# Optimization experiments

Hardware: AMD Instinct MI355X
Metric: run time of the kernel (lower is better)

## Reference

```python
import jax, jax.numpy as jnp
import numpy as np
import math

EMBED_DIM = 2048
NUM_HEADS = 16
HEAD_DIM = EMBED_DIM // NUM_HEADS
BATCH = 2
SEQ = 2048


def setup_inputs() -> dict:
    key = jax.random.key(0)
    ks = jax.random.split(key, 6)
    scale = 1.0 / math.sqrt(EMBED_DIM)
    x = jax.random.normal(ks[0], (BATCH, SEQ, EMBED_DIM), dtype=jnp.float32)
    mask = jnp.ones((BATCH, SEQ), dtype=jnp.float32)
    Wq = jax.random.normal(ks[1], (EMBED_DIM, EMBED_DIM), dtype=jnp.float32) * scale
    Wk = jax.random.normal(ks[2], (EMBED_DIM, EMBED_DIM), dtype=jnp.float32) * scale
    Wv = jax.random.normal(ks[3], (EMBED_DIM, EMBED_DIM), dtype=jnp.float32) * scale
    Wo = jax.random.normal(ks[4], (EMBED_DIM, EMBED_DIM), dtype=jnp.float32) * scale
    return {"x": x, "mask": mask, "Wq": Wq, "Wk": Wk, "Wv": Wv, "Wo": Wo}


def _rope(q, k, seq_len):
    # q, k: [B, H, S, D]
    d = q.shape[-1]
    position = jnp.arange(seq_len, dtype=jnp.float32)[:, None]          # [S,1]
    freqs = 1.0 / (10000.0 ** (jnp.arange(0, d, 2, dtype=jnp.float32) / d))  # [D/2]
    angles = position * freqs                                            # [S,D/2]
    sin = jnp.concatenate([jnp.sin(angles), jnp.sin(angles)], axis=-1)[None, None]  # [1,1,S,D]
    cos = jnp.concatenate([jnp.cos(angles), jnp.cos(angles)], axis=-1)[None, None]

    def rotate_half(t):
        t1, t2 = jnp.split(t, 2, axis=-1)
        return jnp.concatenate([-t2, t1], axis=-1)

    q = q * cos + rotate_half(q) * sin
    k = k * cos + rotate_half(k) * sin
    return q, k


def reference(x, mask, Wq, Wk, Wv, Wo):
    B, S, E = x.shape
    H, D = NUM_HEADS, HEAD_DIM
    # nn.Linear(y) = y @ W.T
    q = (x @ Wq.T).reshape(B, S, H, D).transpose(0, 2, 1, 3)  # [B,H,S,D]
    k = (x @ Wk.T).reshape(B, S, H, D).transpose(0, 2, 1, 3)
    v = (x @ Wv.T).reshape(B, S, H, D).transpose(0, 2, 1, 3)
    q, k = _rope(q, k, S)
    scores = jnp.einsum('bhqd,bhkd->bhqk', q, k) / math.sqrt(D)  # [B,H,S,S]
    # causal mask (strict upper triangle -> -inf)
    causal = jnp.triu(jnp.full((S, S), -jnp.inf, dtype=scores.dtype), k=1)
    scores = scores + causal[None, None]
    # padding mask: [B,S] -> [B,1,1,S] over keys
    scores = scores + (1.0 - mask)[:, None, None, :] * -1e9
    attn = jax.nn.softmax(scores, axis=-1)
    context = jnp.einsum('bhqk,bhkd->bhqd', attn, v)  # [B,H,S,D]
    context = context.transpose(0, 2, 1, 3).reshape(B, S, E)
    return context @ Wo.T
```

## Files before the change

### kernel.cpp

```cpp
#include <hip/hip_runtime.h>
#include <math.h>

typedef unsigned short u16;
typedef __attribute__((ext_vector_type(8))) short bf16x8;
typedef __attribute__((ext_vector_type(8))) unsigned short u16x8;
typedef __attribute__((ext_vector_type(4))) float f32x4;

#define MFMA(a, b, c) __builtin_amdgcn_mfma_f32_16x16x32_bf16((a), (b), (c), 0, 0, 0)

#define GLOAD_LDS16(g, l)                                                     \
  __builtin_amdgcn_global_load_lds(                                           \
      (const __attribute__((address_space(1))) void*)(g),                     \
      (__attribute__((address_space(3))) void*)(l), 16, 0, 0)

#define DRAIN_VMEM() asm volatile("s_waitcnt vmcnt(0)" ::: "memory")
#define FENCE_LDS()                                                            \
  do {                                                                         \
    asm volatile("s_waitcnt lgkmcnt(0)" ::: "memory");                         \
    __builtin_amdgcn_sched_barrier(0);                                         \
  } while (0)

__device__ __forceinline__ float bf2f(u16 u) {
  union { unsigned int i; float f; } x; x.i = ((unsigned int)u) << 16; return x.f;
}
__device__ __forceinline__ u16 f2bf(float f) {
  union { float f; unsigned int i; } x; x.f = f;
  unsigned int r = x.i + 0x7FFFu + ((x.i >> 16) & 1u);
  return (u16)(r >> 16);
}

__global__ __launch_bounds__(256) void probe_all(const u16* p0, const u16* p1,
                                                 const u16* p2, const u16* p3,
                                                 const u16* p4, const u16* p5,
                                                 int* __restrict__ flags) {
  const u16* ps[6] = {p0, p1, p2, p3, p4, p5};
  const u16* p = ps[blockIdx.x];
  __shared__ int cnt;
  if (threadIdx.x == 0) cnt = 0;
  __syncthreads();
  const u16 u = p[threadIdx.x * 2];
  const int e = (u >> 7) & 0xFF;
  atomicAdd(&cnt, (e >= 110 && e <= 135) ? 1 : 0);
  __syncthreads();
  if (threadIdx.x == 0) flags[blockIdx.x] = (cnt > 128) ? 1 : 0;
}

__global__ __launch_bounds__(256) void convert_to_bf16(const void* __restrict__ in,
                                                       u16* __restrict__ out, int n8,
                                                       const int* __restrict__ flag) {
  const int i = blockIdx.x * 256 + threadIdx.x;
  if (i >= n8) return;
  if (*flag) {
    ((u16x8*)out)[i] = ((const u16x8*)in)[i];
  } else {
    const float* f = (const float*)in + (size_t)i * 8;
    u16x8 r;
#pragma unroll
    for (int j = 0; j < 8; ++j) r[j] = f2bf(f[j]);
    ((u16x8*)out)[i] = r;
  }
}

__global__ __launch_bounds__(256) void build_mexp(const void* __restrict__ mask,
                                                  const int* __restrict__ mflag,
                                                  float* __restrict__ mexp, int n) {
  const int i = blockIdx.x * 256 + threadIdx.x;
  if (i >= n) return;
  const float m = *mflag ? bf2f(((const u16*)mask)[i]) : ((const float*)mask)[i];
  mexp[i] = (1.0f - m) * -1e9f;
}

__global__ __launch_bounds__(256) void gemm_bt(const u16* __restrict__ A,
                                               const u16* __restrict__ B,
                                               void* __restrict__ dst,
                                               int K, int mode) {
  __shared__ __align__(16) u16 As[2][128 * 64];
  __shared__ __align__(16) u16 Bs[2][128 * 64];
  const int tid  = threadIdx.x;
  const int wave = tid >> 6, lane = tid & 63;
  const int quad = lane >> 4, m16 = lane & 15;
  const int wm = (wave >> 1) * 64, wn = (wave & 1) * 64;
  const size_t bi = (size_t)blockIdx.y * 128;
  const size_t bj = (size_t)blockIdx.x * 128;

  f32x4 acc[4][4];
  const f32x4 fz = {0.f, 0.f, 0.f, 0.f};
#pragma unroll
  for (int i = 0; i < 4; ++i)
#pragma unroll
    for (int j = 0; j < 4; ++j) acc[i][j] = fz;

  const u16* gA[4]; const u16* gB[4]; int lofs[4];
#pragma unroll
  for (int j = 0; j < 4; ++j) {
    const int t  = (wave * 4 + j) * 64 + lane;
    const int r  = t >> 3;
    const int cs = t & 7;
    const int c  = cs ^ (r & 7);
    gA[j] = A + (bi + r) * (size_t)K + c * 8;
    gB[j] = B + (bj + r) * (size_t)K + c * 8;
    lofs[j] = t * 8;
  }

#pragma unroll
  for (int j = 0; j < 4; ++j) GLOAD_LDS16(gA[j], &As[0][lofs[j]]);
#pragma unroll
  for (int j = 0; j < 4; ++j) GLOAD_LDS16(gB[j], &Bs[0][lofs[j]]);

  const int nIter = K >> 6;
  for (int it = 0; it < nIter; ++it) {
    DRAIN_VMEM();
    __syncthreads();
    if (it + 1 < nIter) {
      const int ko = (it + 1) << 6;
      const int nb = (it + 1) & 1;
#pragma unroll
      for (int j = 0; j < 4; ++j) GLOAD_LDS16(gA[j] + ko, &As[nb][lofs[j]]);
#pragma unroll
      for (int j = 0; j < 4; ++j) GLOAD_LDS16(gB[j] + ko, &Bs[nb][lofs[j]]);
    }
    const int cb = it & 1;

    bf16x8 af[2][4], bfv[2][4];
#pragma unroll
    for (int kk = 0; kk < 2; ++kk) {
#pragma unroll
      for (int mt = 0; mt < 4; ++mt) {
        const int m = wm + mt * 16 + m16;
        af[kk][mt] = *(const bf16x8*)&As[cb][m * 64 + ((kk * 4 + quad) ^ (m & 7)) * 8];
      }
#pragma unroll
      for (int nt = 0; nt < 4; ++nt) {
        const int n = wn + nt * 16 + m16;
        bfv[kk][nt] = *(const bf16x8*)&Bs[cb][n * 64 + ((kk * 4 + quad) ^ (n & 7)) * 8];
      }
    }
#pragma unroll
    for (int kk = 0; kk < 2; ++kk)
#pragma unroll
      for (int mt = 0; mt < 4; ++mt)
#pragma unroll
        for (int nt = 0; nt < 4; ++nt)
          acc[mt][nt] = MFMA(af[kk][mt], bfv[kk][nt], acc[mt][nt]);
  }

#pragma unroll
  for (int mt = 0; mt < 4; ++mt) {
#pragma unroll
    for (int nt = 0; nt < 4; ++nt) {
#pragma unroll
      for (int rg = 0; rg < 4; ++rg) {
        const int row = (int)bi + wm + mt * 16 + quad * 4 + rg;
        const int col = (int)bj + wn + nt * 16 + m16;
        const float v = acc[mt][nt][rg];
        if (mode == 2) {
          ((float*)dst)[(size_t)row * 2048 + col] = v;
        } else {
          const int bb = row >> 11, s = row & 2047, hh = col >> 7, dd = col & 127;
          const size_t idx =
              (mode == 0) ? ((((size_t)bb * 16 + hh) * 2048 + s) * 128 + dd)
                          : ((((size_t)bb * 16 + hh) * 128 + dd) * 2048 + s);
          ((u16*)dst)[idx] = f2bf(v);
        }
      }
    }
  }
}

__global__ __launch_bounds__(256) void rope_kernel(u16* __restrict__ Qr,
                                                   u16* __restrict__ Kr) {
  const int tid = blockIdx.x * 256 + threadIdx.x;
  const int j  = tid & 63;
  const int s  = (tid >> 6) & 2047;
  const int bh = tid >> 17;
  const size_t base = ((size_t)bh * 2048 + s) * 128;
  const float freq = __expf(-(float)j * (9.2103403719761836f / 64.0f));
  float sn, cs;
  sincosf((float)s * freq, &sn, &cs);
  const float qs = 0.08838834764831845f;
  const float q1 = bf2f(Qr[base + j]), q2 = bf2f(Qr[base + j + 64]);
  Qr[base + j]      = f2bf((q1 * cs - q2 * sn) * qs);
  Qr[base + j + 64] = f2bf((q2 * cs + q1 * sn) * qs);
  const float k1 = bf2f(Kr[base + j]), k2 = bf2f(Kr[base + j + 64]);
  Kr[base + j]      = f2bf(k1 * cs - k2 * sn);
  Kr[base + j + 64] = f2bf(k2 * cs + k1 * sn);
}

__global__ __launch_bounds__(256, 2) void flash_attn(const u16* __restrict__ Q,
                                                     const u16* __restrict__ Kg,
                                                     const u16* __restrict__ Vg,
                                                     const float* __restrict__ mexp_g,
                                                     u16* __restrict__ ctx) {
  const int S = 2048, D = 128;
  __shared__ __align__(16) u16 Kt[2][64 * 128];
  __shared__ __align__(16) u16 Vt[2][128 * 64];
  __shared__ __align__(16) u16 Pt[128 * 64];
  const int tid  = threadIdx.x;
  const int wave = tid >> 6, lane = tid & 63;
  const int quad = lane >> 4, m16 = lane & 15;
  const int qtile = 15 - (int)blockIdx.x;
  const int q0 = qtile * 128;
  const int bh = blockIdx.y;
  const int b = bh >> 4, h = bh & 15;
  const size_t baseQK = (size_t)bh * S * D;
  const size_t baseV  = (size_t)bh * D * S;

  const u16* gK[4]; const u16* gV[4]; int lK[4], lV[4];
#pragma unroll
  for (int j = 0; j < 4; ++j) {
    const int t = (wave * 4 + j) * 64 + lane;
    {
      const int r = t >> 4, cs = t & 15;
      const int c = (cs & 8) | ((cs ^ r) & 7);
      gK[j] = Kg + baseQK + (size_t)r * D + c * 8;
      lK[j] = t * 8;
    }
    {
      const int d = t >> 3, cs = t & 7;
      const int c = cs ^ (d & 7);
      gV[j] = Vg + baseV + (size_t)d * S + c * 8;
      lV[j] = t * 8;
    }
  }

  bf16x8 qf[2][4];
#pragma unroll
  for (int st = 0; st < 2; ++st)
#pragma unroll
    for (int kb = 0; kb < 4; ++kb)
      qf[st][kb] = *(const bf16x8*)&Q[baseQK +
          (size_t)(q0 + wave * 32 + st * 16 + m16) * D + kb * 32 + quad * 8];

  float li[2][4] = {{0.f, 0.f, 0.f, 0.f}, {0.f, 0.f, 0.f, 0.f}};
  f32x4 oacc[2][8];
  const f32x4 fz = {0.f, 0.f, 0.f, 0.f};
#pragma unroll
  for (int st = 0; st < 2; ++st)
#pragma unroll
    for (int dt = 0; dt < 8; ++dt) oacc[st][dt] = fz;

#pragma unroll
  for (int j = 0; j < 4; ++j) GLOAD_LDS16(gK[j], &Kt[0][lK[j]]);
#pragma unroll
  for (int j = 0; j < 4; ++j) GLOAD_LDS16(gV[j], &Vt[0][lV[j]]);

  const int ktmax = 2 * qtile + 1;
  for (int kt = 0; kt <= ktmax; ++kt) {
    const int k0 = kt * 64;
    const int cb = kt & 1;
    DRAIN_VMEM();
    __syncthreads();

    float madd[4];
#pragma unroll
    for (int nt = 0; nt < 4; ++nt)
      madd[nt] = mexp_g[b * S + k0 + nt * 16 + m16];

    if (kt < ktmax) {
      const int nb = 1 - cb;
#pragma unroll
      for (int j = 0; j < 4; ++j) GLOAD_LDS16(gK[j] + (size_t)(k0 + 64) * D, &Kt[nb][lK[j]]);
#pragma unroll
      for (int j = 0; j < 4; ++j) GLOAD_LDS16(gV[j] + (k0 + 64), &Vt[nb][lV[j]]);
    }

#pragma unroll
    for (int st = 0; st < 2; ++st) {
      f32x4 sacc[4];
#pragma unroll
      for (int nt = 0; nt < 4; ++nt) sacc[nt] = fz;
#pragma unroll
      for (int nt = 0; nt < 4; ++nt)
#pragma unroll
        for (int kb = 0; kb < 4; ++kb) {
          const int c = kb * 4 + quad;
          const int cs = (c & 8) | ((c ^ m16) & 7);
          bf16x8 kf = *(const bf16x8*)&Kt[cb][(nt * 16 + m16) * 128 + cs * 8];
          sacc[nt] = MFMA(qf[st][kb], kf, sacc[nt]);
        }

      const int R0   = q0 + wave * 32 + st * 16;
      const int prow = wave * 32 + st * 16 + quad * 4;
      if (k0 + 63 > R0) {
#pragma unroll
        for (int rg = 0; rg < 4; ++rg) {
          const int row = R0 + quad * 4 + rg;
          const int pr  = prow + rg;
          float ps = 0.f;
#pragma unroll
          for (int nt = 0; nt < 4; ++nt) {
            const int col = k0 + nt * 16 + m16;
            const float p = (col > row) ? 0.f : __expf(sacc[nt][rg] + madd[nt]);
            ps += p;
            const int c = nt * 2 + (m16 >> 3);
            Pt[pr * 64 + ((c ^ pr) & 7) * 8 + (m16 & 7)] = f2bf(p);
          }
          li[st][rg] += ps;
        }
      } else {
#pragma unroll
        for (int rg = 0; rg < 4; ++rg) {
          const int pr = prow + rg;
          float ps = 0.f;
#pragma unroll
          for (int nt = 0; nt < 4; ++nt) {
            const float p = __expf(sacc[nt][rg] + madd[nt]);
            ps += p;
            const int c = nt * 2 + (m16 >> 3);
            Pt[pr * 64 + ((c ^ pr) & 7) * 8 + (m16 & 7)] = f2bf(p);
          }
          li[st][rg] += ps;
        }
      }
    }
    FENCE_LDS();

#pragma unroll
    for (int kb = 0; kb < 2; ++kb) {
      const int c = kb * 4 + quad;
      const int cs = (c ^ m16) & 7;
      bf16x8 pf0 = *(const bf16x8*)&Pt[(wave * 32 + m16) * 64 + cs * 8];
      bf16x8 pf1 = *(const bf16x8*)&Pt[(wave * 32 + 16 + m16) * 64 + cs * 8];
#pragma unroll
      for (int dt = 0; dt < 8; ++dt) {
        bf16x8 vf = *(const bf16x8*)&Vt[cb][(dt * 16 + m16) * 64 + cs * 8];
        oacc[0][dt] = MFMA(pf0, vf, oacc[0][dt]);
        oacc[1][dt] = MFMA(pf1, vf, oacc[1][dt]);
      }
    }
  }

#pragma unroll
  for (int st = 0; st < 2; ++st) {
#pragma unroll
    for (int rg = 0; rg < 4; ++rg) {
      float ls = li[st][rg];
#pragma unroll
      for (int mk = 1; mk < 16; mk <<= 1) ls += __shfl_xor(ls, mk, 64);
      const float inv = 1.0f / ls;
      const int srow = q0 + wave * 32 + st * 16 + quad * 4 + rg;
#pragma unroll
      for (int dt = 0; dt < 8; ++dt) {
        const int e = h * 128 + dt * 16 + m16;
        ctx[((size_t)b * S + srow) * 2048 + e] = f2bf(oacc[st][dt][rg] * inv);
      }
    }
  }
}

extern "C" void kernel_launch(void* const* d_in, const int* in_sizes, int n_in,
                              void* d_out, int out_size, void* d_ws, size_t ws_size,
                              hipStream_t stream) {
  (void)in_sizes; (void)n_in; (void)out_size; (void)ws_size;
  const int Bz = 2, S = 2048, E = 2048, H = 16, M = Bz * S;
  const size_t NX = (size_t)Bz * S * E;
  const size_t NW = (size_t)E * E;
  const size_t NM = (size_t)Bz * S;

  char* ws = (char*)d_ws;
  int*   flags = (int*)ws;
  float* mexp  = (float*)(ws + 256);
  u16* xc  = (u16*)(ws + 256 + 16384);
  u16* Wqc = xc + NX;
  u16* Wkc = Wqc + NW;
  u16* Wvc = Wkc + NW;
  u16* Woc = Wvc + NW;
  u16* Qr  = Woc + NW;
  u16* Kr  = Qr + NX;
  u16* Vt  = Kr + NX;
  u16* ctx = Vt + NX;

  probe_all<<<6, 256, 0, stream>>>((const u16*)d_in[0], (const u16*)d_in[1],
                                   (const u16*)d_in[2], (const u16*)d_in[3],
                                   (const u16*)d_in[4], (const u16*)d_in[5], flags);

  convert_to_bf16<<<(int)(NX / 8 / 256), 256, 0, stream>>>(d_in[0], xc,  (int)(NX / 8), flags + 0);
  convert_to_bf16<<<(int)(NW / 8 / 256), 256, 0, stream>>>(d_in[2], Wqc, (int)(NW / 8), flags + 2);
  convert_to_bf16<<<(int)(NW / 8 / 256), 256, 0, stream>>>(d_in[3], Wkc, (int)(NW / 8), flags + 3);
  convert_to_bf16<<<(int)(NW / 8 / 256), 256, 0, stream>>>(d_in[4], Wvc, (int)(NW / 8), flags + 4);
  convert_to_bf16<<<(int)(NW / 8 / 256), 256, 0, stream>>>(d_in[5], Woc, (int)(NW / 8), flags + 5);
  build_mexp<<<16, 256, 0, stream>>>(d_in[1], flags + 1, mexp, (int)NM);

  dim3 ggrid(E / 128, M / 128);
  gemm_bt<<<ggrid, 256, 0, stream>>>(xc, Wqc, Qr, E, 0);
  gemm_bt<<<ggrid, 256, 0, stream>>>(xc, Wkc, Kr, E, 0);
  gemm_bt<<<ggrid, 256, 0, stream>>>(xc, Wvc, Vt, E, 1);
  rope_kernel<<<(Bz * H * S * 64) / 256, 256, 0, stream>>>(Qr, Kr);
  flash_attn<<<dim3(16, Bz * H), 256, 0, stream>>>(Qr, Kr, Vt, mexp, ctx);
  gemm_bt<<<ggrid, 256, 0, stream>>>(ctx, Woc, d_out, E, 2);
}
```

Baseline: 439.7 us.

## Fuse input conversions and QKV GEMMs; restructure flash attention into balanced paired passes

Merges the five bf16 conversions and the mask build into one prep kernel. It also fuses the Q, K and V projections into a single GEMM launch over a concatenated weight matrix, with band-dependent output layout. Flash attention now gives each block two 64-row query halves from complementary tiles (a high and a low tile) to balance causal work. It also single-buffers V, with V loads overlapping the QK MFMA, and shrinks LDS use. The aim is fewer launches, better load balance and better occupancy, at the cost of less V prefetch depth.

```diff
diff --git a/kernel.cpp b/kernel.cpp
--- a/kernel.cpp
+++ b/kernel.cpp
@@ -45,29 +45,43 @@
   if (threadIdx.x == 0) flags[blockIdx.x] = (cnt > 128) ? 1 : 0;
 }
 
-__global__ __launch_bounds__(256) void convert_to_bf16(const void* __restrict__ in,
-                                                       u16* __restrict__ out, int n8,
-                                                       const int* __restrict__ flag) {
-  const int i = blockIdx.x * 256 + threadIdx.x;
-  if (i >= n8) return;
-  if (*flag) {
-    ((u16x8*)out)[i] = ((const u16x8*)in)[i];
+__global__ __launch_bounds__(256) void prep_all(const void* __restrict__ x_in,
+                                                const void* __restrict__ wq_in,
+                                                const void* __restrict__ wk_in,
+                                                const void* __restrict__ wv_in,
+                                                const void* __restrict__ wo_in,
+                                                const void* __restrict__ mask_in,
+                                                u16* __restrict__ xc,
+                                                float* __restrict__ mexp,
+                                                const int* __restrict__ flags) {
+  const int blk = blockIdx.x;
+  if (blk < 12288) {
+    const int i = blk * 256 + threadIdx.x;
+    const void* in; u16* out; int fi, off;
+    if (i < (1 << 20)) {
+      in = x_in; out = xc; fi = 0; off = i;
+    } else {
+      const int k = i - (1 << 20);
+      const int seg = k >> 19;
+      off = k & ((1 << 19) - 1);
+      in = (seg == 0) ? wq_in : (seg == 1) ? wk_in : (seg == 2) ? wv_in : wo_in;
+      out = xc + ((size_t)1 << 23) + ((size_t)seg << 22);
+      fi = 2 + seg;
+    }
+    if (flags[fi]) {
+      ((u16x8*)out)[off] = ((const u16x8*)in)[off];
+    } else {
+      const float* f = (const float*)in + (size_t)off * 8;
+      u16x8 r;
+#pragma unroll
+      for (int j = 0; j < 8; ++j) r[j] = f2bf(f[j]);
+      ((u16x8*)out)[off] = r;
+    }
   } else {
-    const float* f = (const float*)in + (size_t)i * 8;
-    u16x8 r;
-#pragma unroll
-    for (int j = 0; j < 8; ++j) r[j] = f2bf(f[j]);
-    ((u16x8*)out)[i] = r;
-  }
-}
-
-__global__ __launch_bounds__(256) void build_mexp(const void* __restrict__ mask,
-                                                  const int* __restrict__ mflag,
-                                                  float* __restrict__ mexp, int n) {
-  const int i = blockIdx.x * 256 + threadIdx.x;
-  if (i >= n) return;
-  const float m = *mflag ? bf2f(((const u16*)mask)[i]) : ((const float*)mask)[i];
-  mexp[i] = (1.0f - m) * -1e9f;
+    const int i = (blk - 12288) * 256 + threadIdx.x;
+    const float m = flags[1] ? bf2f(((const u16*)mask_in)[i]) : ((const float*)mask_in)[i];
+    mexp[i] = (1.0f - m) * -1e9f;
+  }
 }
 
 __global__ __launch_bounds__(256) void gemm_bt(const u16* __restrict__ A,
@@ -156,10 +170,12 @@
         if (mode == 2) {
           ((float*)dst)[(size_t)row * 2048 + col] = v;
         } else {
-          const int bb = row >> 11, s = row & 2047, hh = col >> 7, dd = col & 127;
-          const size_t idx =
-              (mode == 0) ? ((((size_t)bb * 16 + hh) * 2048 + s) * 128 + dd)
-                          : ((((size_t)bb * 16 + hh) * 128 + dd) * 2048 + s);
+          const int band = col >> 11, lc = col & 2047;
+          const int bb = row >> 11, s = row & 2047, hh = lc >> 7, dd = lc & 127;
+          const size_t bandbase = (size_t)band * 8388608u;
+          const size_t idx = (band == 2)
+              ? bandbase + ((((size_t)bb * 16 + hh) * 128 + dd) * 2048 + s)
+              : bandbase + ((((size_t)bb * 16 + hh) * 2048 + s) * 128 + dd);
           ((u16*)dst)[idx] = f2bf(v);
         }
       }
@@ -193,13 +209,13 @@
                                                      u16* __restrict__ ctx) {
   const int S = 2048, D = 128;
   __shared__ __align__(16) u16 Kt[2][64 * 128];
-  __shared__ __align__(16) u16 Vt[2][128 * 64];
-  __shared__ __align__(16) u16 Pt[128 * 64];
+  __shared__ __align__(16) u16 Vt[128 * 64];
+  __shared__ __align__(16) u16 Pt[64 * 64];
   const int tid  = threadIdx.x;
   const int wave = tid >> 6, lane = tid & 63;
   const int quad = lane >> 4, m16 = lane & 15;
-  const int qtile = 15 - (int)blockIdx.x;
-  const int q0 = qtile * 128;
+  const int px = blockIdx.x >> 1;
+  const int hl = blockIdx.x & 1;
   const int bh = blockIdx.y;
   const int b = bh >> 4, h = bh & 15;
   const size_t baseQK = (size_t)bh * S * D;
@@ -223,49 +239,47 @@
     }
   }
 
-  bf16x8 qf[2][4];
-#pragma unroll
-  for (int st = 0; st < 2; ++st)
+  const f32x4 fz = {0.f, 0.f, 0.f, 0.f};
+
+  for (int pass = 0; pass < 2; ++pass) {
+    const int qtile = pass ? px : 15 - px;
+    const int q0 = qtile * 128 + hl * 64;
+    const int ktmax = 2 * qtile + hl;
+
+    __syncthreads();
+
+    bf16x8 qf[4];
 #pragma unroll
     for (int kb = 0; kb < 4; ++kb)
-      qf[st][kb] = *(const bf16x8*)&Q[baseQK +
-          (size_t)(q0 + wave * 32 + st * 16 + m16) * D + kb * 32 + quad * 8];
-
-  float li[2][4] = {{0.f, 0.f, 0.f, 0.f}, {0.f, 0.f, 0.f, 0.f}};
-  f32x4 oacc[2][8];
-  const f32x4 fz = {0.f, 0.f, 0.f, 0.f};
-#pragma unroll
-  for (int st = 0; st < 2; ++st)
-#pragma unroll
-    for (int dt = 0; dt < 8; ++dt) oacc[st][dt] = fz;
-
-#pragma unroll
-  for (int j = 0; j < 4; ++j) GLOAD_LDS16(gK[j], &Kt[0][lK[j]]);
-#pragma unroll
-  for (int j = 0; j < 4; ++j) GLOAD_LDS16(gV[j], &Vt[0][lV[j]]);
-
-  const int ktmax = 2 * qtile + 1;
-  for (int kt = 0; kt <= ktmax; ++kt) {
-    const int k0 = kt * 64;
-    const int cb = kt & 1;
-    DRAIN_VMEM();
-    __syncthreads();
-
-    float madd[4];
-#pragma unroll
-    for (int nt = 0; nt < 4; ++nt)
-      madd[nt] = mexp_g[b * S + k0 + nt * 16 + m16];
-
-    if (kt < ktmax) {
-      const int nb = 1 - cb;
-#pragma unroll
-      for (int j = 0; j < 4; ++j) GLOAD_LDS16(gK[j] + (size_t)(k0 + 64) * D, &Kt[nb][lK[j]]);
-#pragma unroll
-      for (int j = 0; j < 4; ++j) GLOAD_LDS16(gV[j] + (k0 + 64), &Vt[nb][lV[j]]);
-    }
-
-#pragma unroll
-    for (int st = 0; st < 2; ++st) {
+      qf[kb] = *(const bf16x8*)&Q[baseQK +
+          (size_t)(q0 + wave * 16 + m16) * D + kb * 32 + quad * 8];
+
+    float li[4] = {0.f, 0.f, 0.f, 0.f};
+    f32x4 oacc[8];
+#pragma unroll
+    for (int dt = 0; dt < 8; ++dt) oacc[dt] = fz;
+
+#pragma unroll
+    for (int j = 0; j < 4; ++j) GLOAD_LDS16(gK[j], &Kt[0][lK[j]]);
+
+    for (int kt = 0; kt <= ktmax; ++kt) {
+      const int k0 = kt * 64;
+      const int cb = kt & 1;
+      DRAIN_VMEM();
+      __syncthreads();
+
+#pragma unroll
+      for (int j = 0; j < 4; ++j) GLOAD_LDS16(gV[j] + k0, &Vt[lV[j]]);
+      float madd[4];
+#pragma unroll
+      for (int nt = 0; nt < 4; ++nt)
+        madd[nt] = mexp_g[b * S + k0 + nt * 16 + m16];
+      if (kt < ktmax) {
+#pragma unroll
+        for (int j = 0; j < 4; ++j)
+          GLOAD_LDS16(gK[j] + (size_t)(k0 + 64) * D, &Kt[cb ^ 1][lK[j]]);
+      }
+
       f32x4 sacc[4];
 #pragma unroll
       for (int nt = 0; nt < 4; ++nt) sacc[nt] = fz;
@@ -276,11 +290,15 @@
           const int c = kb * 4 + quad;
           const int cs = (c & 8) | ((c ^ m16) & 7);
           bf16x8 kf = *(const bf16x8*)&Kt[cb][(nt * 16 + m16) * 128 + cs * 8];
-          sacc[nt] = MFMA(qf[st][kb], kf, sacc[nt]);
-        }
-
-      const int R0   = q0 + wave * 32 + st * 16;
-      const int prow = wave * 32 + st * 16 + quad * 4;
+          sacc[nt] = MFMA(qf[kb], kf, sacc[nt]);
+        }
+
+      if (kt < ktmax) { asm volatile("s_waitcnt vmcnt(4)" ::: "memory"); }
+      else           { asm volatile("s_waitcnt vmcnt(0)" ::: "memory"); }
+      __builtin_amdgcn_sched_barrier(0);
+
+      const int R0   = q0 + wave * 16;
+      const int prow = wave * 16 + quad * 4;
       if (k0 + 63 > R0) {
 #pragma unroll
         for (int rg = 0; rg < 4; ++rg) {
@@ -295,7 +313,7 @@
             const int c = nt * 2 + (m16 >> 3);
             Pt[pr * 64 + ((c ^ pr) & 7) * 8 + (m16 & 7)] = f2bf(p);
           }
-          li[st][rg] += ps;
+          li[rg] += ps;
         }
       } else {
 #pragma unroll
@@ -309,40 +327,35 @@
             const int c = nt * 2 + (m16 >> 3);
             Pt[pr * 64 + ((c ^ pr) & 7) * 8 + (m16 & 7)] = f2bf(p);
           }
-          li[st][rg] += ps;
-        }
-      }
-    }
-    FENCE_LDS();
-
-#pragma unroll
-    for (int kb = 0; kb < 2; ++kb) {
-      const int c = kb * 4 + quad;
-      const int cs = (c ^ m16) & 7;
-      bf16x8 pf0 = *(const bf16x8*)&Pt[(wave * 32 + m16) * 64 + cs * 8];
-      bf16x8 pf1 = *(const bf16x8*)&Pt[(wave * 32 + 16 + m16) * 64 + cs * 8];
-#pragma unroll
-      for (int dt = 0; dt < 8; ++dt) {
-        bf16x8 vf = *(const bf16x8*)&Vt[cb][(dt * 16 + m16) * 64 + cs * 8];
-        oacc[0][dt] = MFMA(pf0, vf, oacc[0][dt]);
-        oacc[1][dt] = MFMA(pf1, vf, oacc[1][dt]);
-      }
-    }
-  }
-
-#pragma unroll
-  for (int st = 0; st < 2; ++st) {
+          li[rg] += ps;
+        }
+      }
+      FENCE_LDS();
+
+#pragma unroll
+      for (int kb = 0; kb < 2; ++kb) {
+        const int c = kb * 4 + quad;
+        const int cs = (c ^ m16) & 7;
+        bf16x8 pf = *(const bf16x8*)&Pt[(wave * 16 + m16) * 64 + cs * 8];
+#pragma unroll
+        for (int dt = 0; dt < 8; ++dt) {
+          bf16x8 vf = *(const bf16x8*)&Vt[(dt * 16 + m16) * 64 + cs * 8];
+          oacc[dt] = MFMA(pf, vf, oacc[dt]);
+        }
+      }
+    }
+
 #pragma unroll
     for (int rg = 0; rg < 4; ++rg) {
-      float ls = li[st][rg];
+      float ls = li[rg];
 #pragma unroll
       for (int mk = 1; mk < 16; mk <<= 1) ls += __shfl_xor(ls, mk, 64);
       const float inv = 1.0f / ls;
-      const int srow = q0 + wave * 32 + st * 16 + quad * 4 + rg;
+      const int srow = q0 + wave * 16 + quad * 4 + rg;
 #pragma unroll
       for (int dt = 0; dt < 8; ++dt) {
         const int e = h * 128 + dt * 16 + m16;
-        ctx[((size_t)b * S + srow) * 2048 + e] = f2bf(oacc[st][dt][rg] * inv);
+        ctx[((size_t)b * S + srow) * 2048 + e] = f2bf(oacc[dt][rg] * inv);
       }
     }
   }
@@ -355,37 +368,27 @@
   const int Bz = 2, S = 2048, E = 2048, H = 16, M = Bz * S;
   const size_t NX = (size_t)Bz * S * E;
   const size_t NW = (size_t)E * E;
-  const size_t NM = (size_t)Bz * S;
 
   char* ws = (char*)d_ws;
   int*   flags = (int*)ws;
   float* mexp  = (float*)(ws + 256);
   u16* xc  = (u16*)(ws + 256 + 16384);
   u16* Wqc = xc + NX;
-  u16* Wkc = Wqc + NW;
-  u16* Wvc = Wkc + NW;
-  u16* Woc = Wvc + NW;
-  u16* Qr  = Woc + NW;
+  u16* Qr  = Wqc + 4 * NW;
   u16* Kr  = Qr + NX;
   u16* Vt  = Kr + NX;
   u16* ctx = Vt + NX;
+  u16* Woc = Wqc + 3 * NW;
 
   probe_all<<<6, 256, 0, stream>>>((const u16*)d_in[0], (const u16*)d_in[1],
                                    (const u16*)d_in[2], (const u16*)d_in[3],
                                    (const u16*)d_in[4], (const u16*)d_in[5], flags);
 
-  convert_to_bf16<<<(int)(NX / 8 / 256), 256, 0, stream>>>(d_in[0], xc,  (int)(NX / 8), flags + 0);
-  convert_to_bf16<<<(int)(NW / 8 / 256), 256, 0, stream>>>(d_in[2], Wqc, (int)(NW / 8), flags + 2);
-  convert_to_bf16<<<(int)(NW / 8 / 256), 256, 0, stream>>>(d_in[3], Wkc, (int)(NW / 8), flags + 3);
-  convert_to_bf16<<<(int)(NW / 8 / 256), 256, 0, stream>>>(d_in[4], Wvc, (int)(NW / 8), flags + 4);
-  convert_to_bf16<<<(int)(NW / 8 / 256), 256, 0, stream>>>(d_in[5], Woc, (int)(NW / 8), flags + 5);
-  build_mexp<<<16, 256, 0, stream>>>(d_in[1], flags + 1, mexp, (int)NM);
-
-  dim3 ggrid(E / 128, M / 128);
-  gemm_bt<<<ggrid, 256, 0, stream>>>(xc, Wqc, Qr, E, 0);
-  gemm_bt<<<ggrid, 256, 0, stream>>>(xc, Wkc, Kr, E, 0);
-  gemm_bt<<<ggrid, 256, 0, stream>>>(xc, Wvc, Vt, E, 1);
+  prep_all<<<12304, 256, 0, stream>>>(d_in[0], d_in[2], d_in[3], d_in[4],
+                                      d_in[5], d_in[1], xc, mexp, flags);
+
+  gemm_bt<<<dim3(48, 32), 256, 0, stream>>>(xc, Wqc, Qr, E, 3);
   rope_kernel<<<(Bz * H * S * 64) / 256, 256, 0, stream>>>(Qr, Kr);
   flash_attn<<<dim3(16, Bz * H), 256, 0, stream>>>(Qr, Kr, Vt, mexp, ctx);
-  gemm_bt<<<ggrid, 256, 0, stream>>>(ctx, Woc, d_out, E, 2);
-}
+  gemm_bt<<<dim3(16, 32), 256, 0, stream>>>(ctx, Woc, d_out, E, 2);
+}
```

After: 418.1 us. -4.9%, faster.
